# Optimization experiments

Measured on AMD Instinct MI355X. Metric: run time of the kernel, lower is better.

The kernel has to match this reference:

```python
import jax, jax.numpy as jnp
import numpy as np

N_RES = 256
D_PAIR = 128
NUM_HEADS = 16
D_HEAD = 32
D_INNER = NUM_HEADS * D_HEAD  # 512


def setup_inputs() -> dict:
    key = jax.random.key(0)
    ks = jax.random.split(key, 5)
    s_in = 1.0 / np.sqrt(D_PAIR)
    s_out = 1.0 / np.sqrt(D_INNER)
    return {
        "pair_repr": jax.random.normal(ks[0], (N_RES, N_RES, D_PAIR), jnp.float32),
        "Wq": jax.random.normal(ks[1], (D_PAIR, D_INNER), jnp.float32) * s_in,
        "bq": jnp.zeros((D_INNER,), jnp.float32),
        "Wk": jax.random.normal(ks[2], (D_PAIR, D_INNER), jnp.float32) * s_in,
        "bk": jnp.zeros((D_INNER,), jnp.float32),
        "Wv": jax.random.normal(ks[3], (D_PAIR, D_INNER), jnp.float32) * s_in,
        "bv": jnp.zeros((D_INNER,), jnp.float32),
        "Wo": jax.random.normal(ks[4], (D_INNER, D_PAIR), jnp.float32) * s_out,
        "bo": jnp.zeros((D_PAIR,), jnp.float32),
    }


def reference(pair_repr, Wq, bq, Wk, bk, Wv, bv, Wo, bo):
    N = pair_repr.shape[0]
    # Projections -> (N, N, H, Dh)
    q = (pair_repr @ Wq + bq).reshape(N, N, NUM_HEADS, D_HEAD)
    k = (pair_repr @ Wk + bk).reshape(N, N, NUM_HEADS, D_HEAD)
    v = (pair_repr @ Wv + bv).reshape(N, N, NUM_HEADS, D_HEAD)
    # Triangular attention for starting nodes: attend over k index per row i.
    a = jnp.einsum('ijhc,ikhc->ijkh', q, k) / jnp.sqrt(jnp.asarray(D_HEAD, q.dtype))
    # Lower-triangular mask over (j, k), broadcast over (i, h).
    mask = jnp.tril(jnp.ones((N, N), dtype=bool))[None, :, :, None]
    a = jnp.where(mask, a, jnp.asarray(-1e9, a.dtype))
    a = jax.nn.softmax(a, axis=2)
    o = jnp.einsum('ijkh,ikhc->ijhc', a, v).reshape(N, N, D_INNER)
    return pair_repr + (o @ Wo + bo)
```

## Files before the change

### kernel.cpp

```cpp
#include <hip/hip_runtime.h>
#include <hip/hip_bf16.h>

#define NRES 256
#define DPAIR 128
#define NHEADS 16
#define DHEAD 32
#define DINNER 512

typedef unsigned short u16;
typedef __attribute__((ext_vector_type(4))) float f32x4;
typedef __attribute__((ext_vector_type(8))) short s16x8;
typedef __attribute__((ext_vector_type(4))) short s16x4;

#define QSCALE (0.17677669529663687f * 1.4426950408889634f)

__device__ __forceinline__ u16 f32_to_bf16(float f) {
    unsigned int u = __builtin_bit_cast(unsigned int, f);
    unsigned int r = (u + 0x7FFFu + ((u >> 16) & 1u)) >> 16;
    return (u16)r;
}

__device__ __forceinline__ float fast_exp2(float x) {
#if __has_builtin(__builtin_amdgcn_exp2f)
    return __builtin_amdgcn_exp2f(x);
#else
    return exp2f(x);
#endif
}

__device__ __forceinline__ f32x4 mfma_16x16x16_bf16(s16x4 a, s16x4 b, f32x4 c) {
#if __has_builtin(__builtin_amdgcn_mfma_f32_16x16x16bf16_1k)
    return __builtin_amdgcn_mfma_f32_16x16x16bf16_1k(a, b, c, 0, 0, 0);
#elif __has_builtin(__builtin_amdgcn_mfma_f32_16x16x16_bf16)
    return __builtin_amdgcn_mfma_f32_16x16x16_bf16(a, b, c, 0, 0, 0);
#else
    f32x4 d;
    asm volatile("v_mfma_f32_16x16x16_bf16 %0, %1, %2, %3"
                 : "=v"(d) : "v"(a), "v"(b), "v"(c));
    return d;
#endif
}

__device__ __forceinline__ void gll16(const void* g, void* l) {
    __builtin_amdgcn_global_load_lds(
        (__attribute__((address_space(1))) unsigned int*)(uintptr_t)g,
        (__attribute__((address_space(3))) unsigned int*)(unsigned int)(uintptr_t)l,
        16, 0, 0);
}

__global__ __launch_bounds__(256) void prep_pair(const float* __restrict__ pair,
                                                 u16* __restrict__ pairb) {
    const int id = blockIdx.x * 256 + threadIdx.x;
    const float4* s = reinterpret_cast<const float4*>(pair) + (size_t)id * 2;
    const float4 v0 = s[0], v1 = s[1];
    ushort4 lo, hi;
    lo.x = f32_to_bf16(v0.x); lo.y = f32_to_bf16(v0.y);
    lo.z = f32_to_bf16(v0.z); lo.w = f32_to_bf16(v0.w);
    hi.x = f32_to_bf16(v1.x); hi.y = f32_to_bf16(v1.y);
    hi.z = f32_to_bf16(v1.z); hi.w = f32_to_bf16(v1.w);
    ushort4* d = reinterpret_cast<ushort4*>(pairb + (size_t)id * 8);
    d[0] = lo; d[1] = hi;
}

__global__ __launch_bounds__(256) void wconv(const float* __restrict__ Wq,
                                             const float* __restrict__ Wk,
                                             const float* __restrict__ Wv,
                                             const float* __restrict__ Wo,
                                             u16* wq_t, u16* wk_t, u16* wv_t, u16* wo_t) {
    int id = blockIdx.x * 256 + threadIdx.x;
    if (id < 3 * 65536) {
        int m = id / 65536;
        int e = id % 65536;
        int k = e >> 9, n = e & 511;
        const float* W = (m == 0) ? Wq : ((m == 1) ? Wk : Wv);
        u16* Wt = (m == 0) ? wq_t : ((m == 1) ? wk_t : wv_t);
        Wt[n * 128 + k] = f32_to_bf16(W[e]);
    } else {
        int e = id - 3 * 65536;
        int k = e >> 7, n = e & 127;
        wo_t[n * 512 + k] = f32_to_bf16(Wo[e]);
    }
}

__global__ __launch_bounds__(512, 2) void fused_attn(const u16* __restrict__ pairb,
                                                     const u16* __restrict__ wq_t,
                                                     const u16* __restrict__ wk_t,
                                                     const u16* __restrict__ wv_t,
                                                     const float* __restrict__ bq,
                                                     const float* __restrict__ bk,
                                                     const float* __restrict__ bv,
                                                     u16* __restrict__ o_ws) {
    __shared__ u16 pairS[256 * 128];
    __shared__ u16 wS[3 * 32 * 128];
    __shared__ u16 qS[256 * 40];
    __shared__ u16 kS[256 * 40];
    __shared__ u16 vTS[32 * 264];

    const int bx = ((blockIdx.x & 7) << 9) | (blockIdx.x >> 3);
    const int i = bx >> 4, h = bx & 15;
    const int tid = threadIdx.x;
    const int wave = tid >> 6, lane = tid & 63;
    const int g = lane >> 4, l15 = lane & 15;

    {
        const char* pb = (const char*)(pairb + (size_t)i * 256 * 128);
        for (int it = 0; it < 8; ++it) {
            const int chunk = wave * 8 + it;
            const int row = chunk * 4 + (lane >> 4);
            const int col = (lane & 15) ^ (row & 7);
            gll16(pb + row * 256 + col * 16, (void*)(pairS + chunk * 512));
        }
        for (int it = 0; it < 3; ++it) {
            const int chunk = wave * 3 + it;
            const int m = chunk >> 3;
            const int lc = chunk & 7;
            const u16* Wt = (m == 0) ? wq_t : ((m == 1) ? wk_t : wv_t);
            const int c = lc * 4 + (lane >> 4);
            const int col = (lane & 15) ^ (c & 7);
            gll16((const char*)(Wt + (size_t)(h * 32) * 128) + c * 256 + col * 16,
                  (void*)(wS + (m * 32 + lc * 4) * 128));
        }
    }
    __syncthreads();

    {
        const int j0 = wave * 32;
        f32x4 aq[2][2], ak[2][2], av[2][2];
        for (int a = 0; a < 2; ++a)
            for (int b = 0; b < 2; ++b) {
                aq[a][b] = f32x4{0.f, 0.f, 0.f, 0.f};
                ak[a][b] = f32x4{0.f, 0.f, 0.f, 0.f};
                av[a][b] = f32x4{0.f, 0.f, 0.f, 0.f};
            }
        for (int kk = 0; kk < 4; ++kk) {
            s16x8 pf[2], wf[3][2];
            for (int jf = 0; jf < 2; ++jf) {
                const int row = j0 + jf * 16 + l15;
                const int ch = (kk * 4 + g) ^ (row & 7);
                pf[jf] = *reinterpret_cast<s16x8*>(&pairS[row * 128 + ch * 8]);
            }
            for (int m = 0; m < 3; ++m)
                for (int cf = 0; cf < 2; ++cf) {
                    const int c = cf * 16 + l15;
                    const int ch = (kk * 4 + g) ^ (c & 7);
                    wf[m][cf] = *reinterpret_cast<s16x8*>(&wS[(m * 32 + c) * 128 + ch * 8]);
                }
            for (int cf = 0; cf < 2; ++cf)
                for (int jf = 0; jf < 2; ++jf) {
                    aq[cf][jf] = __builtin_amdgcn_mfma_f32_16x16x32_bf16(wf[0][cf], pf[jf], aq[cf][jf], 0, 0, 0);
                    ak[cf][jf] = __builtin_amdgcn_mfma_f32_16x16x32_bf16(wf[1][cf], pf[jf], ak[cf][jf], 0, 0, 0);
                    av[jf][cf] = __builtin_amdgcn_mfma_f32_16x16x32_bf16(pf[jf], wf[2][cf], av[jf][cf], 0, 0, 0);
                }
        }
        for (int cf = 0; cf < 2; ++cf) {
            const int c = cf * 16 + g * 4;
            const float4 b4q = *reinterpret_cast<const float4*>(bq + h * 32 + c);
            const float4 b4k = *reinterpret_cast<const float4*>(bk + h * 32 + c);
            for (int jf = 0; jf < 2; ++jf) {
                const int j = j0 + jf * 16 + l15;
                ushort4 oq, ok;
                oq.x = f32_to_bf16((aq[cf][jf][0] + b4q.x) * QSCALE);
                oq.y = f32_to_bf16((aq[cf][jf][1] + b4q.y) * QSCALE);
                oq.z = f32_to_bf16((aq[cf][jf][2] + b4q.z) * QSCALE);
                oq.w = f32_to_bf16((aq[cf][jf][3] + b4q.w) * QSCALE);
                *reinterpret_cast<ushort4*>(&qS[j * 40 + c]) = oq;
                ok.x = f32_to_bf16(ak[cf][jf][0] + b4k.x);
                ok.y = f32_to_bf16(ak[cf][jf][1] + b4k.y);
                ok.z = f32_to_bf16(ak[cf][jf][2] + b4k.z);
                ok.w = f32_to_bf16(ak[cf][jf][3] + b4k.w);
                *reinterpret_cast<ushort4*>(&kS[j * 40 + c]) = ok;
            }
        }
        for (int cf = 0; cf < 2; ++cf) {
            const int c = cf * 16 + l15;
            const float bvv = bv[h * 32 + c];
            for (int jf = 0; jf < 2; ++jf) {
                const int j = j0 + jf * 16 + g * 4;
                ushort4 ov;
                ov.x = f32_to_bf16(av[jf][cf][0] + bvv);
                ov.y = f32_to_bf16(av[jf][cf][1] + bvv);
                ov.z = f32_to_bf16(av[jf][cf][2] + bvv);
                ov.w = f32_to_bf16(av[jf][cf][3] + bvv);
                *reinterpret_cast<ushort4*>(&vTS[c * 264 + j]) = ov;
            }
        }
    }
    __syncthreads();

    const size_t obase = ((size_t)i * 256) * 512 + h * 32;

    for (int ch2 = 0; ch2 < 2; ++ch2) {
        const int t = (ch2 == 0) ? wave : (15 - wave);
        const int jbase = t * 16;
        const int ktmax = t + 1;

        const s16x8 qf = *reinterpret_cast<const s16x8*>(&qS[(jbase + l15) * 40 + g * 8]);

        f32x4 o0 = {0.f, 0.f, 0.f, 0.f}, o1 = {0.f, 0.f, 0.f, 0.f};
        float sum = 0.f;

        for (int kt = 0; kt < ktmax; ++kt) {
            const s16x8 kf = *reinterpret_cast<s16x8*>(&kS[(kt * 16 + l15) * 40 + g * 8]);
            f32x4 s = __builtin_amdgcn_mfma_f32_16x16x32_bf16(kf, qf, f32x4{0.f, 0.f, 0.f, 0.f}, 0, 0, 0);
            float p0, p1, p2, p3;
            if (kt == t) {
                p0 = ((g * 4 + 0) > l15) ? 0.f : fast_exp2(s[0]);
                p1 = ((g * 4 + 1) > l15) ? 0.f : fast_exp2(s[1]);
                p2 = ((g * 4 + 2) > l15) ? 0.f : fast_exp2(s[2]);
                p3 = ((g * 4 + 3) > l15) ? 0.f : fast_exp2(s[3]);
            } else {
                p0 = fast_exp2(s[0]); p1 = fast_exp2(s[1]);
                p2 = fast_exp2(s[2]); p3 = fast_exp2(s[3]);
            }
            sum += (p0 + p1) + (p2 + p3);
            unsigned e0 = __builtin_bit_cast(unsigned, p0) + 0x8000u;
            unsigned e1 = __builtin_bit_cast(unsigned, p1) + 0x8000u;
            unsigned e2 = __builtin_bit_cast(unsigned, p2) + 0x8000u;
            unsigned e3 = __builtin_bit_cast(unsigned, p3) + 0x8000u;
            uint2 pw;
            pw.x = __builtin_amdgcn_perm(e1, e0, 0x07060302u);
            pw.y = __builtin_amdgcn_perm(e3, e2, 0x07060302u);
            const s16x4 pb = __builtin_bit_cast(s16x4, pw);
            const s16x4 va0 = *reinterpret_cast<s16x4*>(&vTS[l15 * 264 + kt * 16 + g * 4]);
            const s16x4 va1 = *reinterpret_cast<s16x4*>(&vTS[(16 + l15) * 264 + kt * 16 + g * 4]);
            o0 = mfma_16x16x16_bf16(va0, pb, o0);
            o1 = mfma_16x16x16_bf16(va1, pb, o1);
        }

        sum += __shfl_xor(sum, 16, 64);
        sum += __shfl_xor(sum, 32, 64);
        const float rinv = 1.0f / sum;

        unsigned x0 = __builtin_bit_cast(unsigned, o0[0] * rinv) + 0x8000u;
        unsigned x1 = __builtin_bit_cast(unsigned, o0[1] * rinv) + 0x8000u;
        unsigned x2 = __builtin_bit_cast(unsigned, o0[2] * rinv) + 0x8000u;
        unsigned x3 = __builtin_bit_cast(unsigned, o0[3] * rinv) + 0x8000u;
        uint2 w0;
        w0.x = __builtin_amdgcn_perm(x1, x0, 0x07060302u);
        w0.y = __builtin_amdgcn_perm(x3, x2, 0x07060302u);
        unsigned y0 = __builtin_bit_cast(unsigned, o1[0] * rinv) + 0x8000u;
        unsigned y1 = __builtin_bit_cast(unsigned, o1[1] * rinv) + 0x8000u;
        unsigned y2 = __builtin_bit_cast(unsigned, o1[2] * rinv) + 0x8000u;
        unsigned y3 = __builtin_bit_cast(unsigned, o1[3] * rinv) + 0x8000u;
        uint2 w1;
        w1.x = __builtin_amdgcn_perm(y1, y0, 0x07060302u);
        w1.y = __builtin_amdgcn_perm(y3, y2, 0x07060302u);

        u16* orow = o_ws + obase + (size_t)(jbase + l15) * 512;
        *reinterpret_cast<uint2*>(orow + g * 4) = w0;
        *reinterpret_cast<uint2*>(orow + 16 + g * 4) = w1;
    }
}

__global__ __launch_bounds__(256) void outproj(const u16* __restrict__ o_ws,
                                               const u16* __restrict__ wo_t,
                                               const float* __restrict__ pair,
                                               const float* __restrict__ bo,
                                               float* __restrict__ out) {
    __shared__ u16 As[64 * 72];
    __shared__ u16 Bs[128 * 72];
    const int tid = threadIdx.x;
    const int m0 = blockIdx.x * 64;
    const int wave = tid >> 6, lane = tid & 63;
    const int g = lane >> 4, l15 = lane & 15;

    f32x4 acc[8];
    for (int c = 0; c < 8; ++c) acc[c] = f32x4{0.f, 0.f, 0.f, 0.f};

    for (int kt = 0; kt < 8; ++kt) {
        __syncthreads();
        for (int it = 0; it < 2; ++it) {
            int L = tid + it * 256;
            int row = L >> 3, seg = L & 7;
            *reinterpret_cast<s16x8*>(&As[row * 72 + seg * 8]) =
                *reinterpret_cast<const s16x8*>(o_ws + (size_t)(m0 + row) * 512 + kt * 64 + seg * 8);
        }
        for (int it = 0; it < 4; ++it) {
            int L = tid + it * 256;
            int n = L >> 3, seg = L & 7;
            *reinterpret_cast<s16x8*>(&Bs[n * 72 + seg * 8]) =
                *reinterpret_cast<const s16x8*>(wo_t + (size_t)n * 512 + kt * 64 + seg * 8);
        }
        __syncthreads();
        for (int kk = 0; kk < 2; ++kk) {
            const s16x8 a = *reinterpret_cast<s16x8*>(&As[(wave * 16 + l15) * 72 + kk * 32 + g * 8]);
            for (int c = 0; c < 8; ++c) {
                const s16x8 b = *reinterpret_cast<s16x8*>(&Bs[(c * 16 + l15) * 72 + kk * 32 + g * 8]);
                acc[c] = __builtin_amdgcn_mfma_f32_16x16x32_bf16(a, b, acc[c], 0, 0, 0);
            }
        }
    }

    for (int c = 0; c < 8; ++c) {
        const int n = c * 16 + l15;
        const float bias = bo[n];
        for (int r = 0; r < 4; ++r) {
            const size_t row = m0 + wave * 16 + g * 4 + r;
            out[row * 128 + n] = acc[c][r] + bias + pair[row * 128 + n];
        }
    }
}

extern "C" void kernel_launch(void* const* d_in, const int* in_sizes, int n_in,
                              void* d_out, int out_size, void* d_ws, size_t ws_size,
                              hipStream_t stream) {
    const float* pair = (const float*)d_in[0];
    const float* Wq = (const float*)d_in[1];
    const float* bq = (const float*)d_in[2];
    const float* Wk = (const float*)d_in[3];
    const float* bk = (const float*)d_in[4];
    const float* Wv = (const float*)d_in[5];
    const float* bv = (const float*)d_in[6];
    const float* Wo = (const float*)d_in[7];
    const float* bo = (const float*)d_in[8];
    float* out = (float*)d_out;

    char* ws = (char*)d_ws;
    u16* o_ws  = (u16*)(ws);
    u16* wq_t  = (u16*)(ws + 67108864);
    u16* wk_t  = wq_t + 65536;
    u16* wv_t  = wk_t + 65536;
    u16* wo_t  = wv_t + 65536;
    u16* pairb = (u16*)(ws + 67108864 + 1048576);

    wconv<<<1024, 256, 0, stream>>>(Wq, Wk, Wv, Wo, wq_t, wk_t, wv_t, wo_t);
    prep_pair<<<4096, 256, 0, stream>>>(pair, pairb);
    fused_attn<<<4096, 512, 0, stream>>>(pairb, wq_t, wk_t, wv_t, bq, bk, bv, o_ws);
    outproj<<<1024, 256, 0, stream>>>(o_ws, wo_t, pair, bo, out);
}
```

Baseline: 136.8 us.

## Drop pair LDS staging, load pair rows to registers, dual-accumulate attention loop

```diff
diff --git a/kernel.cpp b/kernel.cpp
--- a/kernel.cpp
+++ b/kernel.cpp
@@ -82,7 +82,7 @@
     }
 }
 
-__global__ __launch_bounds__(512, 2) void fused_attn(const u16* __restrict__ pairb,
+__global__ __launch_bounds__(512, 4) void fused_attn(const u16* __restrict__ pairb,
                                                      const u16* __restrict__ wq_t,
                                                      const u16* __restrict__ wk_t,
                                                      const u16* __restrict__ wv_t,
@@ -90,9 +90,8 @@
                                                      const float* __restrict__ bk,
                                                      const float* __restrict__ bv,
                                                      u16* __restrict__ o_ws) {
-    __shared__ u16 pairS[256 * 128];
     __shared__ u16 wS[3 * 32 * 128];
-    __shared__ u16 qS[256 * 40];
+    __shared__ u16 qS[256 * 32];
     __shared__ u16 kS[256 * 40];
     __shared__ u16 vTS[32 * 264];
 
@@ -101,61 +100,65 @@
     const int tid = threadIdx.x;
     const int wave = tid >> 6, lane = tid & 63;
     const int g = lane >> 4, l15 = lane & 15;
-
+    const int j0 = wave * 32;
+
+    for (int it = 0; it < 3; ++it) {
+        const int chunk = wave * 3 + it;
+        const int m = chunk >> 3;
+        const int lc = chunk & 7;
+        const u16* Wt = (m == 0) ? wq_t : ((m == 1) ? wk_t : wv_t);
+        const int c = lc * 4 + (lane >> 4);
+        const int col = (lane & 15) ^ (c & 7);
+        gll16((const char*)(Wt + (size_t)(h * 32) * 128) + c * 256 + col * 16,
+              (void*)(wS + (m * 32 + lc * 4) * 128));
+    }
+    s16x8 pf[2][4];
     {
-        const char* pb = (const char*)(pairb + (size_t)i * 256 * 128);
-        for (int it = 0; it < 8; ++it) {
-            const int chunk = wave * 8 + it;
-            const int row = chunk * 4 + (lane >> 4);
-            const int col = (lane & 15) ^ (row & 7);
-            gll16(pb + row * 256 + col * 16, (void*)(pairS + chunk * 512));
-        }
-        for (int it = 0; it < 3; ++it) {
-            const int chunk = wave * 3 + it;
-            const int m = chunk >> 3;
-            const int lc = chunk & 7;
-            const u16* Wt = (m == 0) ? wq_t : ((m == 1) ? wk_t : wv_t);
-            const int c = lc * 4 + (lane >> 4);
-            const int col = (lane & 15) ^ (c & 7);
-            gll16((const char*)(Wt + (size_t)(h * 32) * 128) + c * 256 + col * 16,
-                  (void*)(wS + (m * 32 + lc * 4) * 128));
-        }
+        const u16* prow = pairb + (size_t)(i * 256 + j0 + l15) * 128;
+        #pragma unroll
+        for (int jf = 0; jf < 2; ++jf)
+            #pragma unroll
+            for (int kk = 0; kk < 4; ++kk)
+                pf[jf][kk] = *reinterpret_cast<const s16x8*>(prow + jf * 16 * 128 + kk * 32 + g * 8);
     }
     __syncthreads();
 
     {
-        const int j0 = wave * 32;
         f32x4 aq[2][2], ak[2][2], av[2][2];
+        #pragma unroll
         for (int a = 0; a < 2; ++a)
+            #pragma unroll
             for (int b = 0; b < 2; ++b) {
                 aq[a][b] = f32x4{0.f, 0.f, 0.f, 0.f};
                 ak[a][b] = f32x4{0.f, 0.f, 0.f, 0.f};
                 av[a][b] = f32x4{0.f, 0.f, 0.f, 0.f};
             }
+        #pragma unroll
         for (int kk = 0; kk < 4; ++kk) {
-            s16x8 pf[2], wf[3][2];
-            for (int jf = 0; jf < 2; ++jf) {
-                const int row = j0 + jf * 16 + l15;
-                const int ch = (kk * 4 + g) ^ (row & 7);
-                pf[jf] = *reinterpret_cast<s16x8*>(&pairS[row * 128 + ch * 8]);
-            }
+            s16x8 wf[3][2];
+            #pragma unroll
             for (int m = 0; m < 3; ++m)
+                #pragma unroll
                 for (int cf = 0; cf < 2; ++cf) {
                     const int c = cf * 16 + l15;
                     const int ch = (kk * 4 + g) ^ (c & 7);
                     wf[m][cf] = *reinterpret_cast<s16x8*>(&wS[(m * 32 + c) * 128 + ch * 8]);
                 }
+            #pragma unroll
             for (int cf = 0; cf < 2; ++cf)
+                #pragma unroll
                 for (int jf = 0; jf < 2; ++jf) {
-                    aq[cf][jf] = __builtin_amdgcn_mfma_f32_16x16x32_bf16(wf[0][cf], pf[jf], aq[cf][jf], 0, 0, 0);
-                    ak[cf][jf] = __builtin_amdgcn_mfma_f32_16x16x32_bf16(wf[1][cf], pf[jf], ak[cf][jf], 0, 0, 0);
-                    av[jf][cf] = __builtin_amdgcn_mfma_f32_16x16x32_bf16(pf[jf], wf[2][cf], av[jf][cf], 0, 0, 0);
+                    aq[cf][jf] = __builtin_amdgcn_mfma_f32_16x16x32_bf16(wf[0][cf], pf[jf][kk], aq[cf][jf], 0, 0, 0);
+                    ak[cf][jf] = __builtin_amdgcn_mfma_f32_16x16x32_bf16(wf[1][cf], pf[jf][kk], ak[cf][jf], 0, 0, 0);
+                    av[jf][cf] = __builtin_amdgcn_mfma_f32_16x16x32_bf16(pf[jf][kk], wf[2][cf], av[jf][cf], 0, 0, 0);
                 }
         }
+        #pragma unroll
         for (int cf = 0; cf < 2; ++cf) {
             const int c = cf * 16 + g * 4;
             const float4 b4q = *reinterpret_cast<const float4*>(bq + h * 32 + c);
             const float4 b4k = *reinterpret_cast<const float4*>(bk + h * 32 + c);
+            #pragma unroll
             for (int jf = 0; jf < 2; ++jf) {
                 const int j = j0 + jf * 16 + l15;
                 ushort4 oq, ok;
@@ -163,7 +166,8 @@
                 oq.y = f32_to_bf16((aq[cf][jf][1] + b4q.y) * QSCALE);
                 oq.z = f32_to_bf16((aq[cf][jf][2] + b4q.z) * QSCALE);
                 oq.w = f32_to_bf16((aq[cf][jf][3] + b4q.w) * QSCALE);
-                *reinterpret_cast<ushort4*>(&qS[j * 40 + c]) = oq;
+                *reinterpret_cast<ushort4*>(
+                    &qS[j * 32 + (((cf << 1) + (g >> 1)) ^ (j & 3)) * 8 + (g & 1) * 4]) = oq;
                 ok.x = f32_to_bf16(ak[cf][jf][0] + b4k.x);
                 ok.y = f32_to_bf16(ak[cf][jf][1] + b4k.y);
                 ok.z = f32_to_bf16(ak[cf][jf][2] + b4k.z);
@@ -171,9 +175,11 @@
                 *reinterpret_cast<ushort4*>(&kS[j * 40 + c]) = ok;
             }
         }
+        #pragma unroll
         for (int cf = 0; cf < 2; ++cf) {
             const int c = cf * 16 + l15;
             const float bvv = bv[h * 32 + c];
+            #pragma unroll
             for (int jf = 0; jf < 2; ++jf) {
                 const int j = j0 + jf * 16 + g * 4;
                 ushort4 ov;
@@ -194,12 +200,14 @@
         const int jbase = t * 16;
         const int ktmax = t + 1;
 
-        const s16x8 qf = *reinterpret_cast<const s16x8*>(&qS[(jbase + l15) * 40 + g * 8]);
-
-        f32x4 o0 = {0.f, 0.f, 0.f, 0.f}, o1 = {0.f, 0.f, 0.f, 0.f};
-        float sum = 0.f;
-
-        for (int kt = 0; kt < ktmax; ++kt) {
+        const s16x8 qf = *reinterpret_cast<const s16x8*>(
+            &qS[(jbase + l15) * 32 + (g ^ (l15 & 3)) * 8]);
+
+        f32x4 oA0 = {0.f, 0.f, 0.f, 0.f}, oA1 = {0.f, 0.f, 0.f, 0.f};
+        f32x4 oB0 = {0.f, 0.f, 0.f, 0.f}, oB1 = {0.f, 0.f, 0.f, 0.f};
+        float sA = 0.f, sB = 0.f;
+
+        auto body = [&](int kt, f32x4& u0, f32x4& u1, float& sm) {
             const s16x8 kf = *reinterpret_cast<s16x8*>(&kS[(kt * 16 + l15) * 40 + g * 8]);
             f32x4 s = __builtin_amdgcn_mfma_f32_16x16x32_bf16(kf, qf, f32x4{0.f, 0.f, 0.f, 0.f}, 0, 0, 0);
             float p0, p1, p2, p3;
@@ -212,7 +220,7 @@
                 p0 = fast_exp2(s[0]); p1 = fast_exp2(s[1]);
                 p2 = fast_exp2(s[2]); p3 = fast_exp2(s[3]);
             }
-            sum += (p0 + p1) + (p2 + p3);
+            sm += (p0 + p1) + (p2 + p3);
             unsigned e0 = __builtin_bit_cast(unsigned, p0) + 0x8000u;
             unsigned e1 = __builtin_bit_cast(unsigned, p1) + 0x8000u;
             unsigned e2 = __builtin_bit_cast(unsigned, p2) + 0x8000u;
@@ -223,13 +231,23 @@
             const s16x4 pb = __builtin_bit_cast(s16x4, pw);
             const s16x4 va0 = *reinterpret_cast<s16x4*>(&vTS[l15 * 264 + kt * 16 + g * 4]);
             const s16x4 va1 = *reinterpret_cast<s16x4*>(&vTS[(16 + l15) * 264 + kt * 16 + g * 4]);
-            o0 = mfma_16x16x16_bf16(va0, pb, o0);
-            o1 = mfma_16x16x16_bf16(va1, pb, o1);
-        }
-
+            u0 = mfma_16x16x16_bf16(va0, pb, u0);
+            u1 = mfma_16x16x16_bf16(va1, pb, u1);
+        };
+
+        int kt = 0;
+        for (; kt + 2 <= ktmax; kt += 2) {
+            body(kt, oA0, oA1, sA);
+            body(kt + 1, oB0, oB1, sB);
+        }
+        if (kt < ktmax) body(kt, oA0, oA1, sA);
+
+        float sum = sA + sB;
         sum += __shfl_xor(sum, 16, 64);
         sum += __shfl_xor(sum, 32, 64);
         const float rinv = 1.0f / sum;
+        const f32x4 o0 = oA0 + oB0;
+        const f32x4 o1 = oA1 + oB1;
 
         unsigned x0 = __builtin_bit_cast(unsigned, o0[0] * rinv) + 0x8000u;
         unsigned x1 = __builtin_bit_cast(unsigned, o0[1] * rinv) + 0x8000u;
```

Measured after the change: 119.0 us. 13.0% less time.
